# Kernel optimization log

Measured on AMD Instinct MI355X. Metric: run time of the kernel, lower is better.

Reference implementation:

```python
import jax, jax.numpy as jnp
import numpy as np

N_EMBD = 768
N_HEAD = 8
HEAD_DIM = N_EMBD // N_HEAD


def setup_inputs() -> dict:
    key = jax.random.key(0)
    k1, k2, k3 = jax.random.split(key, 3)
    B, T, C = 8, 1024, N_EMBD
    x = jax.random.normal(k1, (B, T, C), dtype=jnp.float32)
    # nn.Linear(C, 3C, bias=False): store as [C, 3C] so y = x @ W
    W_attn = jax.random.normal(k2, (C, 3 * C), dtype=jnp.float32) * (1.0 / np.sqrt(C))
    W_proj = jax.random.normal(k3, (C, C), dtype=jnp.float32) * (1.0 / np.sqrt(C))
    return {"x": x, "W_attn": W_attn, "W_proj": W_proj}


def reference(x, W_attn, W_proj):
    B, T, C = x.shape
    qkv = x @ W_attn                      # [B,T,3C]
    q, k, v = jnp.split(qkv, 3, axis=2)
    # [B,T,C] -> [B,H,T,D]
    def heads(t):
        return t.reshape(B, T, N_HEAD, HEAD_DIM).transpose(0, 2, 1, 3)
    q, k, v = heads(q), heads(k), heads(v)
    scale = 1.0 / np.sqrt(HEAD_DIM)
    att = jnp.einsum('bhtd,bhsd->bhts', q, k) * scale  # [B,H,T,T]
    causal = jnp.tril(jnp.ones((T, T), dtype=bool))
    att = jnp.where(causal[None, None], att, -jnp.inf)
    att = jax.nn.softmax(att, axis=-1)
    y = jnp.einsum('bhts,bhsd->bhtd', att, v)          # [B,H,T,D]
    y = y.transpose(0, 2, 1, 3).reshape(B, T, C)
    return y @ W_proj
```

## Files before the change

### kernel.cpp

```cpp
#include <hip/hip_runtime.h>
#include <stdint.h>

#define Bz 8
#define Tz 1024
#define Cz 768
#define Hz 8
#define Dz 96
#define BHz 64
#define Kz 768

typedef __bf16 bf16x8 __attribute__((ext_vector_type(8)));
typedef unsigned short u16x8 __attribute__((ext_vector_type(8)));
typedef float f32x4 __attribute__((ext_vector_type(4)));

__device__ __forceinline__ unsigned short f2bf(float f) {
  union { float f; unsigned int u; } v; v.f = f;
  unsigned int u = v.u;
  return (unsigned short)((u + 0x7fffu + ((u >> 16) & 1u)) >> 16);
}

#if defined(__has_builtin)
#if __has_builtin(__builtin_amdgcn_exp2f)
#define EXP2(x) __builtin_amdgcn_exp2f(x)
#endif
#endif
#ifndef EXP2
#define EXP2(x) __expf((x) * 0.6931471805599453f)
#endif

typedef const __attribute__((address_space(1))) void* gas_ptr;
typedef __attribute__((address_space(3))) void* las_ptr;
__device__ __forceinline__ void gl16(const void* g, void* l) {
  __builtin_amdgcn_global_load_lds((gas_ptr)g, (las_ptr)l, 16, 0, 0);
}

__global__ __launch_bounds__(256) void cast_f32_bf16(const float* __restrict__ in,
                                                     unsigned short* __restrict__ out) {
  int i = (blockIdx.x * 256 + threadIdx.x) * 4;
  float4 v = *(const float4*)(in + i);
  union { unsigned short s[4]; uint2 u; } o;
  o.s[0] = f2bf(v.x); o.s[1] = f2bf(v.y); o.s[2] = f2bf(v.z); o.s[3] = f2bf(v.w);
  *(uint2*)(out + i) = o.u;
}

__global__ __launch_bounds__(256) void transpose_cast(const float* __restrict__ in,
                                                      unsigned short* __restrict__ out,
                                                      int R, int Cc) {
  __shared__ unsigned short t[64][72];
  int bx = blockIdx.x * 64;
  int by = blockIdx.y * 64;
  int tid = threadIdx.x;
#pragma unroll
  for (int i = 0; i < 16; i++) {
    int idx = tid + i * 256;
    int r = idx >> 6, c = idx & 63;
    t[c][r] = f2bf(in[(by + r) * Cc + bx + c]);
  }
  __syncthreads();
#pragma unroll
  for (int i = 0; i < 16; i++) {
    int idx = tid + i * 256;
    int r = idx >> 6, c = idx & 63;
    out[(bx + r) * R + by + c] = t[r][c];
  }
}

template <int MODE>
__global__ __launch_bounds__(256)
void gemm128(const unsigned short* __restrict__ A,
             const unsigned short* __restrict__ Bt,
             unsigned short* __restrict__ obf,
             float* __restrict__ of32) {
  __shared__ unsigned short Asm[128 * 32];
  __shared__ unsigned short Bsm[128 * 32];
  const int tid = threadIdx.x;
  const int wave = tid >> 6, lane = tid & 63;
  const int quad = lane >> 4, l16 = lane & 15;
  const int bm = blockIdx.x, bn = blockIdx.y;
  const int wm = (wave >> 1) * 64, wn = (wave & 1) * 64;

  f32x4 zero = {0.f, 0.f, 0.f, 0.f};
  f32x4 acc[4][4];
#pragma unroll
  for (int i = 0; i < 4; i++)
#pragma unroll
    for (int j = 0; j < 4; j++) acc[i][j] = zero;

  const int rr = lane >> 2, c8 = (lane & 3) * 8;
  const unsigned short* Ag0 = A + (size_t)(bm * 128 + wave * 32 + rr) * Kz + c8;
  const unsigned short* Ag1 = Ag0 + 16 * Kz;
  const unsigned short* Bg0 = Bt + (size_t)(bn * 128 + wave * 32 + rr) * Kz + c8;
  const unsigned short* Bg1 = Bg0 + 16 * Kz;
  unsigned short* lA0 = &Asm[wave * 1024];
  unsigned short* lA1 = lA0 + 512;
  unsigned short* lB0 = &Bsm[wave * 1024];
  unsigned short* lB1 = lB0 + 512;

  for (int k0 = 0; k0 < Kz; k0 += 32) {
    __syncthreads();
    gl16(Ag0 + k0, lA0);
    gl16(Ag1 + k0, lA1);
    gl16(Bg0 + k0, lB0);
    gl16(Bg1 + k0, lB1);
    __syncthreads();
    bf16x8 af[4], bfr[4];
#pragma unroll
    for (int mi = 0; mi < 4; mi++)
      af[mi] = *(const bf16x8*)&Asm[(wm + mi * 16 + l16) * 32 + quad * 8];
#pragma unroll
    for (int ni = 0; ni < 4; ni++)
      bfr[ni] = *(const bf16x8*)&Bsm[(wn + ni * 16 + l16) * 32 + quad * 8];
#pragma unroll
    for (int mi = 0; mi < 4; mi++)
#pragma unroll
      for (int ni = 0; ni < 4; ni++)
        acc[mi][ni] = __builtin_amdgcn_mfma_f32_16x16x32_bf16(af[mi], bfr[ni], acc[mi][ni], 0, 0, 0);
  }

#pragma unroll
  for (int mi = 0; mi < 4; mi++) {
    int row = bm * 128 + wm + mi * 16 + quad * 4;
    if (MODE == 0) {
      int b = row >> 10;
      int t = row & 1023;
#pragma unroll
      for (int ni = 0; ni < 4; ni++) {
        int col = bn * 128 + wn + ni * 16 + l16;
        int which = col / 768;
        int cc = col - which * 768;
        int h = cc / 96;
        int d = cc - h * 96;
        if (which == 2) {
          int base = ((2 * 64 + b * 8 + h) * 96 + d) * 1024 + t;
          union { unsigned short s[4]; uint2 u; } o;
#pragma unroll
          for (int r = 0; r < 4; r++) o.s[r] = f2bf(acc[mi][ni][r]);
          *(uint2*)(obf + base) = o.u;
        } else {
          int base = ((which * 64 + b * 8 + h) * 1024 + t) * 96 + d;
#pragma unroll
          for (int r = 0; r < 4; r++) obf[base + r * 96] = f2bf(acc[mi][ni][r]);
        }
      }
    } else {
#pragma unroll
      for (int ni = 0; ni < 4; ni++) {
        int col = bn * 128 + wn + ni * 16 + l16;
#pragma unroll
        for (int r = 0; r < 4; r++) of32[(row + r) * 768 + col] = acc[mi][ni][r];
      }
    }
  }
}

__global__ __launch_bounds__(256, 2)
void attn(const unsigned short* __restrict__ qkv, unsigned short* __restrict__ y) {
  const int bh = blockIdx.x;
  const int by = blockIdx.y;
  const int q0 = ((by < 4) ? (7 - by) : (by - 4)) * 128;
  const int tid = threadIdx.x;
  const int wave = tid >> 6, lane = tid & 63;
  const int quad = lane >> 4, l16 = lane & 15;
  const int qw0 = q0 + wave * 32;
  const int b = bh >> 3, h = bh & 7;

  const unsigned short* Qh = qkv + bh * Tz * Dz;
  const unsigned short* Kh = qkv + (BHz + bh) * Tz * Dz;
  const unsigned short* Vt = qkv + 2 * BHz * Tz * Dz + bh * Dz * Tz;

  __shared__ unsigned short Vsm[96 * 136];
  __shared__ unsigned short Psm[4 * 32 * 136];
  unsigned short* Pw = Psm + wave * 32 * 136;

  const int vd = tid >> 4;
  const int vc = tid & 15;

  bf16x8 aq[2][3];
#pragma unroll
  for (int mi = 0; mi < 2; mi++)
#pragma unroll
    for (int kd = 0; kd < 3; kd++)
      aq[mi][kd] = *(const bf16x8*)(Qh + (qw0 + mi * 16 + l16) * Dz + kd * 32 + quad * 8);

  f32x4 zero = {0.f, 0.f, 0.f, 0.f};
  f32x4 acc_o[2][6];
#pragma unroll
  for (int mi = 0; mi < 2; mi++)
#pragma unroll
    for (int i = 0; i < 6; i++) acc_o[mi][i] = zero;
  const float NEG = -__builtin_inff();
  float mrow[2][4], lrow[2][4];
#pragma unroll
  for (int mi = 0; mi < 2; mi++)
#pragma unroll
    for (int r = 0; r < 4; r++) { mrow[mi][r] = NEG; lrow[mi][r] = 0.f; }
  const float cs = 0.14724538519872735f;

  for (int s0 = 0; s0 <= q0; s0 += 128) {
    u16x8 vreg[6];
#pragma unroll
    for (int g = 0; g < 6; g++)
      vreg[g] = *(const u16x8*)(Vt + (g * 16 + vd) * Tz + s0 + vc * 8);

    const int srem = qw0 + 31 - s0;
    const int nlim = min(7, srem >> 4);
    const int klim = min(3, srem >> 5);

    f32x4 sacc[2][8];
#pragma unroll
    for (int ni = 0; ni < 8; ni++) {
      if (ni <= nlim) {
        sacc[0][ni] = zero; sacc[1][ni] = zero;
#pragma unroll
        for (int kd = 0; kd < 3; kd++) {
          bf16x8 bk = *(const bf16x8*)(Kh + (s0 + ni * 16 + l16) * Dz + kd * 32 + quad * 8);
          sacc[0][ni] = __builtin_amdgcn_mfma_f32_16x16x32_bf16(aq[0][kd], bk, sacc[0][ni], 0, 0, 0);
          sacc[1][ni] = __builtin_amdgcn_mfma_f32_16x16x32_bf16(aq[1][kd], bk, sacc[1][ni], 0, 0, 0);
        }
      }
    }

#pragma unroll
    for (int mi = 0; mi < 2; mi++) {
      float rmax[4] = {NEG, NEG, NEG, NEG};
#pragma unroll
      for (int ni = 0; ni < 8; ni++) {
        if (ni <= nlim) {
          if (s0 + ni * 16 + 15 > qw0 + mi * 16) {
            const int t_base = qw0 + mi * 16 + quad * 4;
            const int s_abs = s0 + ni * 16 + l16;
#pragma unroll
            for (int r = 0; r < 4; r++)
              if (s_abs > t_base + r) sacc[mi][ni][r] = NEG;
          }
#pragma unroll
          for (int r = 0; r < 4; r++) rmax[r] = fmaxf(rmax[r], sacc[mi][ni][r]);
        }
      }
#pragma unroll
      for (int r = 0; r < 4; r++)
#pragma unroll
        for (int sh = 1; sh < 16; sh <<= 1)
          rmax[r] = fmaxf(rmax[r], __shfl_xor(rmax[r], sh));

      int ok = 1;
#pragma unroll
      for (int r = 0; r < 4; r++) ok &= (rmax[r] <= mrow[mi][r] + 54.0f) ? 1 : 0;
      if (!__all(ok)) {
#pragma unroll
        for (int r = 0; r < 4; r++) {
          float mnew = fmaxf(mrow[mi][r], rmax[r]);
          float alpha = EXP2((mrow[mi][r] - mnew) * cs);
          mrow[mi][r] = mnew;
          lrow[mi][r] *= alpha;
#pragma unroll
          for (int di = 0; di < 6; di++) acc_o[mi][di][r] *= alpha;
        }
      }

      float nmc[4];
#pragma unroll
      for (int r = 0; r < 4; r++) nmc[r] = -mrow[mi][r] * cs;
      float rsum[4] = {0.f, 0.f, 0.f, 0.f};
#pragma unroll
      for (int ni = 0; ni < 8; ni++) {
        if (ni <= nlim) {
#pragma unroll
          for (int r = 0; r < 4; r++) {
            float p = EXP2(fmaf(sacc[mi][ni][r], cs, nmc[r]));
            rsum[r] += p;
            Pw[(mi * 16 + quad * 4 + r) * 136 + ni * 16 + l16] = f2bf(p);
          }
        }
      }
#pragma unroll
      for (int r = 0; r < 4; r++) lrow[mi][r] += rsum[r];
    }

    __syncthreads();
#pragma unroll
    for (int g = 0; g < 6; g++)
      *(u16x8*)&Vsm[(g * 16 + vd) * 136 + vc * 8] = vreg[g];
    __syncthreads();

#pragma unroll
    for (int kc = 0; kc < 4; kc++) {
      if (kc <= klim) {
        bf16x8 ap0 = *(const bf16x8*)&Pw[l16 * 136 + kc * 32 + quad * 8];
        bf16x8 ap1 = *(const bf16x8*)&Pw[(16 + l16) * 136 + kc * 32 + quad * 8];
#pragma unroll
        for (int di = 0; di < 6; di++) {
          bf16x8 bv = *(const bf16x8*)&Vsm[(di * 16 + l16) * 136 + kc * 32 + quad * 8];
          acc_o[0][di] = __builtin_amdgcn_mfma_f32_16x16x32_bf16(ap0, bv, acc_o[0][di], 0, 0, 0);
          acc_o[1][di] = __builtin_amdgcn_mfma_f32_16x16x32_bf16(ap1, bv, acc_o[1][di], 0, 0, 0);
        }
      }
    }
  }

#pragma unroll
  for (int mi = 0; mi < 2; mi++) {
#pragma unroll
    for (int r = 0; r < 4; r++) {
#pragma unroll
      for (int sh = 1; sh < 16; sh <<= 1)
        lrow[mi][r] += __shfl_xor(lrow[mi][r], sh);
      float linv = 1.f / lrow[mi][r];
      int t = qw0 + mi * 16 + quad * 4 + r;
#pragma unroll
      for (int di = 0; di < 6; di++) {
        int d = di * 16 + l16;
        y[(b * Tz + t) * Cz + h * Dz + d] = f2bf(acc_o[mi][di][r] * linv);
      }
    }
  }
}

#define OFF_XB   0u
#define OFF_WAT  12582912u
#define OFF_WPT  16121856u
#define OFF_QKV  17301504u
#define OFF_Y    55050240u

extern "C" void kernel_launch(void* const* d_in, const int* in_sizes, int n_in,
                              void* d_out, int out_size, void* d_ws, size_t ws_size,
                              hipStream_t stream) {
  const float* x  = (const float*)d_in[0];
  const float* Wa = (const float*)d_in[1];
  const float* Wp = (const float*)d_in[2];
  float* out = (float*)d_out;
  uint8_t* ws = (uint8_t*)d_ws;
  unsigned short* xb  = (unsigned short*)(ws + OFF_XB);
  unsigned short* Wat = (unsigned short*)(ws + OFF_WAT);
  unsigned short* Wpt = (unsigned short*)(ws + OFF_WPT);
  unsigned short* qkv = (unsigned short*)(ws + OFF_QKV);
  unsigned short* y   = (unsigned short*)(ws + OFF_Y);

  cast_f32_bf16<<<6144, 256, 0, stream>>>(x, xb);
  transpose_cast<<<dim3(36, 12), 256, 0, stream>>>(Wa, Wat, 768, 2304);
  transpose_cast<<<dim3(12, 12), 256, 0, stream>>>(Wp, Wpt, 768, 768);
  gemm128<0><<<dim3(64, 18), 256, 0, stream>>>(xb, Wat, qkv, nullptr);
  attn<<<dim3(64, 8), 256, 0, stream>>>(qkv, y);
  gemm128<1><<<dim3(64, 6), 256, 0, stream>>>(y, Wpt, nullptr, out);
}
```

Measured before the change: 210.3 us.

## Halve attention query tile to 64 rows, raise occupancy, swizzle GEMM blocks

The attention kernel now gives each block 64 query rows (16 per wave) instead of 128, which doubles the grid to 1024 blocks. Launch bounds go from 2 to 3 blocks per SM, and the causal blocks are dispatched longest first. This is meant to improve load balance and occupancy across the CUs. In exchange, each K/V tile is loaded twice as often per query, and a zero-padding write is added for partial P tiles. The GEMM also remaps block indices to group tiles per XCD, aiming for better L2 locality.

```diff
diff --git a/kernel.cpp b/kernel.cpp
--- a/kernel.cpp
+++ b/kernel.cpp
@@ -76,7 +76,10 @@
   const int tid = threadIdx.x;
   const int wave = tid >> 6, lane = tid & 63;
   const int quad = lane >> 4, l16 = lane & 15;
-  const int bm = blockIdx.x, bn = blockIdx.y;
+  const int lin = blockIdx.x + (blockIdx.y << 6);
+  const int cpx = (gridDim.x * gridDim.y) >> 3;
+  const int nl = (lin & 7) * cpx + (lin >> 3);
+  const int bm = nl & 63, bn = nl >> 6;
   const int wm = (wave >> 1) * 64, wn = (wave & 1) * 64;
 
   f32x4 zero = {0.f, 0.f, 0.f, 0.f};
@@ -153,15 +156,15 @@
   }
 }
 
-__global__ __launch_bounds__(256, 2)
+__global__ __launch_bounds__(256, 3)
 void attn(const unsigned short* __restrict__ qkv, unsigned short* __restrict__ y) {
   const int bh = blockIdx.x;
   const int by = blockIdx.y;
-  const int q0 = ((by < 4) ? (7 - by) : (by - 4)) * 128;
+  const int q0 = (15 - by) * 64;
   const int tid = threadIdx.x;
   const int wave = tid >> 6, lane = tid & 63;
   const int quad = lane >> 4, l16 = lane & 15;
-  const int qw0 = q0 + wave * 32;
+  const int qw0 = q0 + wave * 16;
   const int b = bh >> 3, h = bh & 7;
 
   const unsigned short* Qh = qkv + bh * Tz * Dz;
@@ -169,112 +172,109 @@
   const unsigned short* Vt = qkv + 2 * BHz * Tz * Dz + bh * Dz * Tz;
 
   __shared__ unsigned short Vsm[96 * 136];
-  __shared__ unsigned short Psm[4 * 32 * 136];
-  unsigned short* Pw = Psm + wave * 32 * 136;
+  __shared__ unsigned short Psm[4 * 16 * 136];
+  unsigned short* Pw = Psm + wave * 16 * 136;
 
   const int vd = tid >> 4;
   const int vc = tid & 15;
 
-  bf16x8 aq[2][3];
-#pragma unroll
-  for (int mi = 0; mi < 2; mi++)
-#pragma unroll
-    for (int kd = 0; kd < 3; kd++)
-      aq[mi][kd] = *(const bf16x8*)(Qh + (qw0 + mi * 16 + l16) * Dz + kd * 32 + quad * 8);
+  bf16x8 aq[3];
+#pragma unroll
+  for (int kd = 0; kd < 3; kd++)
+    aq[kd] = *(const bf16x8*)(Qh + (qw0 + l16) * Dz + kd * 32 + quad * 8);
 
   f32x4 zero = {0.f, 0.f, 0.f, 0.f};
-  f32x4 acc_o[2][6];
-#pragma unroll
-  for (int mi = 0; mi < 2; mi++)
-#pragma unroll
-    for (int i = 0; i < 6; i++) acc_o[mi][i] = zero;
+  f32x4 acc_o[6];
+#pragma unroll
+  for (int i = 0; i < 6; i++) acc_o[i] = zero;
   const float NEG = -__builtin_inff();
-  float mrow[2][4], lrow[2][4];
-#pragma unroll
-  for (int mi = 0; mi < 2; mi++)
-#pragma unroll
-    for (int r = 0; r < 4; r++) { mrow[mi][r] = NEG; lrow[mi][r] = 0.f; }
+  float mrow[4], lrow[4];
+#pragma unroll
+  for (int r = 0; r < 4; r++) { mrow[r] = NEG; lrow[r] = 0.f; }
   const float cs = 0.14724538519872735f;
 
-  for (int s0 = 0; s0 <= q0; s0 += 128) {
+  const int s_last = (q0 >> 7) << 7;
+  for (int s0 = 0; s0 <= s_last; s0 += 128) {
     u16x8 vreg[6];
 #pragma unroll
     for (int g = 0; g < 6; g++)
       vreg[g] = *(const u16x8*)(Vt + (g * 16 + vd) * Tz + s0 + vc * 8);
 
-    const int srem = qw0 + 31 - s0;
+    const int srem = qw0 + 15 - s0;
     const int nlim = min(7, srem >> 4);
     const int klim = min(3, srem >> 5);
 
-    f32x4 sacc[2][8];
+    f32x4 sacc[8];
 #pragma unroll
     for (int ni = 0; ni < 8; ni++) {
       if (ni <= nlim) {
-        sacc[0][ni] = zero; sacc[1][ni] = zero;
+        sacc[ni] = zero;
 #pragma unroll
         for (int kd = 0; kd < 3; kd++) {
           bf16x8 bk = *(const bf16x8*)(Kh + (s0 + ni * 16 + l16) * Dz + kd * 32 + quad * 8);
-          sacc[0][ni] = __builtin_amdgcn_mfma_f32_16x16x32_bf16(aq[0][kd], bk, sacc[0][ni], 0, 0, 0);
-          sacc[1][ni] = __builtin_amdgcn_mfma_f32_16x16x32_bf16(aq[1][kd], bk, sacc[1][ni], 0, 0, 0);
-        }
-      }
-    }
-
-#pragma unroll
-    for (int mi = 0; mi < 2; mi++) {
-      float rmax[4] = {NEG, NEG, NEG, NEG};
-#pragma unroll
-      for (int ni = 0; ni < 8; ni++) {
-        if (ni <= nlim) {
-          if (s0 + ni * 16 + 15 > qw0 + mi * 16) {
-            const int t_base = qw0 + mi * 16 + quad * 4;
-            const int s_abs = s0 + ni * 16 + l16;
-#pragma unroll
-            for (int r = 0; r < 4; r++)
-              if (s_abs > t_base + r) sacc[mi][ni][r] = NEG;
-          }
-#pragma unroll
-          for (int r = 0; r < 4; r++) rmax[r] = fmaxf(rmax[r], sacc[mi][ni][r]);
-        }
-      }
-#pragma unroll
-      for (int r = 0; r < 4; r++)
-#pragma unroll
-        for (int sh = 1; sh < 16; sh <<= 1)
-          rmax[r] = fmaxf(rmax[r], __shfl_xor(rmax[r], sh));
-
-      int ok = 1;
-#pragma unroll
-      for (int r = 0; r < 4; r++) ok &= (rmax[r] <= mrow[mi][r] + 54.0f) ? 1 : 0;
-      if (!__all(ok)) {
+          sacc[ni] = __builtin_amdgcn_mfma_f32_16x16x32_bf16(aq[kd], bk, sacc[ni], 0, 0, 0);
+        }
+      }
+    }
+
+    float rmax[4] = {NEG, NEG, NEG, NEG};
+#pragma unroll
+    for (int ni = 0; ni < 8; ni++) {
+      if (ni <= nlim) {
+        if (s0 + ni * 16 + 15 > qw0) {
+          const int t_base = qw0 + quad * 4;
+          const int s_abs = s0 + ni * 16 + l16;
+#pragma unroll
+          for (int r = 0; r < 4; r++)
+            if (s_abs > t_base + r) sacc[ni][r] = NEG;
+        }
+#pragma unroll
+        for (int r = 0; r < 4; r++) rmax[r] = fmaxf(rmax[r], sacc[ni][r]);
+      }
+    }
+#pragma unroll
+    for (int r = 0; r < 4; r++)
+#pragma unroll
+      for (int sh = 1; sh < 16; sh <<= 1)
+        rmax[r] = fmaxf(rmax[r], __shfl_xor(rmax[r], sh));
+
+    int ok = 1;
+#pragma unroll
+    for (int r = 0; r < 4; r++) ok &= (rmax[r] <= mrow[r] + 54.0f) ? 1 : 0;
+    if (!__all(ok)) {
+#pragma unroll
+      for (int r = 0; r < 4; r++) {
+        float mnew = fmaxf(mrow[r], rmax[r]);
+        float alpha = EXP2((mrow[r] - mnew) * cs);
+        mrow[r] = mnew;
+        lrow[r] *= alpha;
+#pragma unroll
+        for (int di = 0; di < 6; di++) acc_o[di][r] *= alpha;
+      }
+    }
+
+    float nmc[4];
+#pragma unroll
+    for (int r = 0; r < 4; r++) nmc[r] = -mrow[r] * cs;
+    float rsum[4] = {0.f, 0.f, 0.f, 0.f};
+#pragma unroll
+    for (int ni = 0; ni < 8; ni++) {
+      if (ni <= nlim) {
 #pragma unroll
         for (int r = 0; r < 4; r++) {
-          float mnew = fmaxf(mrow[mi][r], rmax[r]);
-          float alpha = EXP2((mrow[mi][r] - mnew) * cs);
-          mrow[mi][r] = mnew;
-          lrow[mi][r] *= alpha;
-#pragma unroll
-          for (int di = 0; di < 6; di++) acc_o[mi][di][r] *= alpha;
-        }
-      }
-
-      float nmc[4];
-#pragma unroll
-      for (int r = 0; r < 4; r++) nmc[r] = -mrow[mi][r] * cs;
-      float rsum[4] = {0.f, 0.f, 0.f, 0.f};
-#pragma unroll
-      for (int ni = 0; ni < 8; ni++) {
-        if (ni <= nlim) {
-#pragma unroll
-          for (int r = 0; r < 4; r++) {
-            float p = EXP2(fmaf(sacc[mi][ni][r], cs, nmc[r]));
-            rsum[r] += p;
-            Pw[(mi * 16 + quad * 4 + r) * 136 + ni * 16 + l16] = f2bf(p);
-          }
-        }
-      }
-#pragma unroll
-      for (int r = 0; r < 4; r++) lrow[mi][r] += rsum[r];
+          float p = EXP2(fmaf(sacc[ni][r], cs, nmc[r]));
+          rsum[r] += p;
+          Pw[(quad * 4 + r) * 136 + ni * 16 + l16] = f2bf(p);
+        }
+      }
+    }
+#pragma unroll
+    for (int r = 0; r < 4; r++) lrow[r] += rsum[r];
+
+    if (nlim < 7 && !(nlim & 1)) {
+      const int zc = (nlim + 1) * 16 + l16;
+#pragma unroll
+      for (int r = 0; r < 4; r++) Pw[(quad * 4 + r) * 136 + zc] = 0;
     }
 
     __syncthreads();
@@ -286,32 +286,27 @@
 #pragma unroll
     for (int kc = 0; kc < 4; kc++) {
       if (kc <= klim) {
-        bf16x8 ap0 = *(const bf16x8*)&Pw[l16 * 136 + kc * 32 + quad * 8];
-        bf16x8 ap1 = *(const bf16x8*)&Pw[(16 + l16) * 136 + kc * 32 + quad * 8];
+        bf16x8 ap = *(const bf16x8*)&Pw[l16 * 136 + kc * 32 + quad * 8];
 #pragma unroll
         for (int di = 0; di < 6; di++) {
           bf16x8 bv = *(const bf16x8*)&Vsm[(di * 16 + l16) * 136 + kc * 32 + quad * 8];
-          acc_o[0][di] = __builtin_amdgcn_mfma_f32_16x16x32_bf16(ap0, bv, acc_o[0][di], 0, 0, 0);
-          acc_o[1][di] = __builtin_amdgcn_mfma_f32_16x16x32_bf16(ap1, bv, acc_o[1][di], 0, 0, 0);
-        }
-      }
-    }
-  }
-
-#pragma unroll
-  for (int mi = 0; mi < 2; mi++) {
-#pragma unroll
-    for (int r = 0; r < 4; r++) {
-#pragma unroll
-      for (int sh = 1; sh < 16; sh <<= 1)
-        lrow[mi][r] += __shfl_xor(lrow[mi][r], sh);
-      float linv = 1.f / lrow[mi][r];
-      int t = qw0 + mi * 16 + quad * 4 + r;
-#pragma unroll
-      for (int di = 0; di < 6; di++) {
-        int d = di * 16 + l16;
-        y[(b * Tz + t) * Cz + h * Dz + d] = f2bf(acc_o[mi][di][r] * linv);
-      }
+          acc_o[di] = __builtin_amdgcn_mfma_f32_16x16x32_bf16(ap, bv, acc_o[di], 0, 0, 0);
+        }
+      }
+    }
+  }
+
+#pragma unroll
+  for (int r = 0; r < 4; r++) {
+#pragma unroll
+    for (int sh = 1; sh < 16; sh <<= 1)
+      lrow[r] += __shfl_xor(lrow[r], sh);
+    float linv = 1.f / lrow[r];
+    int t = qw0 + quad * 4 + r;
+#pragma unroll
+    for (int di = 0; di < 6; di++) {
+      int d = di * 16 + l16;
+      y[(b * Tz + t) * Cz + h * Dz + d] = f2bf(acc_o[di][r] * linv);
     }
   }
 }
@@ -340,6 +335,6 @@
   transpose_cast<<<dim3(36, 12), 256, 0, stream>>>(Wa, Wat, 768, 2304);
   transpose_cast<<<dim3(12, 12), 256, 0, stream>>>(Wp, Wpt, 768, 768);
   gemm128<0><<<dim3(64, 18), 256, 0, stream>>>(xb, Wat, qkv, nullptr);
-  attn<<<dim3(64, 8), 256, 0, stream>>>(qkv, y);
+  attn<<<dim3(64, 16), 256, 0, stream>>>(qkv, y);
   gemm128<1><<<dim3(64, 6), 256, 0, stream>>>(y, Wpt, nullptr, out);
 }
```

Result: slower. 218.7 us (+4.0%).
